# Kernel optimization log

Measured on AMD Instinct MI355X. Metric: run time of the kernel, lower is better.

## Reference

```python
import jax, jax.numpy as jnp
import numpy as np

ROI_SIZE = 7
SPATIAL_SCALE = 1.0 / 16.0
CHUNK = 16  # rois processed per lax.map step to bound the masked-max intermediate


def roi_pool(x, indices_and_rois):
    """Caffe-style RoI max pooling. x: [N,C,H,W]; indices_and_rois: [R,5]=(idx,x1,y1,x2,y2)."""
    N, C, H, W = x.shape
    P = ROI_SIZE
    hi = jnp.arange(H, dtype=x.dtype)
    wi = jnp.arange(W, dtype=x.dtype)
    p = jnp.arange(P, dtype=x.dtype)

    def pool_one(r5):
        idx = r5[0].astype(jnp.int32)
        xmin, ymin, xmax, ymax = r5[1], r5[2], r5[3], r5[4]
        sw = jnp.round(xmin * SPATIAL_SCALE)
        sh = jnp.round(ymin * SPATIAL_SCALE)
        ew = jnp.round(xmax * SPATIAL_SCALE)
        eh = jnp.round(ymax * SPATIAL_SCALE)
        bw = jnp.maximum(ew - sw + 1.0, 1.0) / P  # bin width in feature cells
        bh = jnp.maximum(eh - sh + 1.0, 1.0) / P
        wstart = jnp.clip(jnp.floor(p * bw) + sw, 0.0, float(W))
        wend = jnp.clip(jnp.ceil((p + 1.0) * bw) + sw, 0.0, float(W))
        hstart = jnp.clip(jnp.floor(p * bh) + sh, 0.0, float(H))
        hend = jnp.clip(jnp.ceil((p + 1.0) * bh) + sh, 0.0, float(H))
        colmask = (wi[None, :] >= wstart[:, None]) & (wi[None, :] < wend[:, None])  # [P,W]
        rowmask = (hi[None, :] >= hstart[:, None]) & (hi[None, :] < hend[:, None])  # [P,H]
        img = x[idx]  # [C,H,W] gather of the roi's image
        neg = jnp.asarray(-jnp.inf, x.dtype)
        # max over columns within each column-bin, then over rows within each row-bin
        m1 = jnp.max(jnp.where(colmask[None, None, :, :], img[:, :, None, :], neg), axis=-1)  # [C,H,P]
        m2 = jnp.max(jnp.where(rowmask[None, :, :, None], m1[:, None, :, :], neg), axis=2)  # [C,P,P]
        return jnp.where(jnp.isfinite(m2), m2, jnp.zeros((), x.dtype))  # empty bins -> 0

    R = indices_and_rois.shape[0]
    chunks = indices_and_rois.reshape(R // CHUNK, CHUNK, 5)
    pooled = jax.lax.map(jax.vmap(pool_one), chunks)  # [R//CHUNK, CHUNK, C, P, P]
    return pooled.reshape(R, C, P, P)


def setup_inputs() -> dict:
    key = jax.random.key(0)
    ks = jax.random.split(key, 8)
    N, C, H, W = 4, 512, 50, 50  # 800x800 image, VGG16 stride 16
    R, n_class = 512, 21
    x = jax.random.normal(ks[0], (N, C, H, W), jnp.float32)
    yx1 = jax.random.uniform(ks[1], (R, 2), jnp.float32, 0.0, 700.0)
    wh = jax.random.uniform(ks[2], (R, 2), jnp.float32, 32.0, 128.0)
    rois = jnp.concatenate([yx1, jnp.minimum(yx1 + wh, 799.0)], axis=1)  # (y1,x1,y2,x2)
    roi_indices = jax.random.randint(ks[3], (R,), 0, N)
    din = C * ROI_SIZE * ROI_SIZE
    W1 = jax.random.normal(ks[4], (din, 4096), jnp.float32) * 0.01
    b1 = jnp.zeros((4096,), jnp.float32)
    W2 = jax.random.normal(ks[5], (4096, 4096), jnp.float32) * 0.01
    b2 = jnp.zeros((4096,), jnp.float32)
    Wc = jax.random.normal(ks[6], (4096, n_class * 4), jnp.float32) * 0.001
    bc = jnp.zeros((n_class * 4,), jnp.float32)
    Ws = jax.random.normal(ks[7], (4096, n_class), jnp.float32) * 0.01
    bs = jnp.zeros((n_class,), jnp.float32)
    return {"x": x, "rois": rois, "roi_indices": roi_indices, "W1": W1, "b1": b1,
            "W2": W2, "b2": b2, "Wc": Wc, "bc": bc, "Ws": Ws, "bs": bs}


def reference(x, rois, roi_indices, W1, b1, W2, b2, Wc, bc, Ws, bs):
    # concat index + boxes, then reorder (idx,y1,x1,y2,x2) -> (idx,x1,y1,x2,y2)
    ir = jnp.concatenate([roi_indices[:, None].astype(jnp.float32), rois], axis=1)
    ir = ir[:, jnp.array([0, 2, 1, 4, 3])]
    pool = roi_pool(x, ir)  # [R, C, 7, 7]
    flat = pool.reshape(pool.shape[0], -1)  # [R, 25088]
    fc6 = jax.nn.relu(flat @ W1 + b1)
    fc7 = jax.nn.relu(fc6 @ W2 + b2)
    roi_cls_locs = fc7 @ Wc + bc  # [R, n_class*4]
    roi_scores = fc7 @ Ws + bs  # [R, n_class]
    return (roi_cls_locs, roi_scores)
```

## Files before the change

### kernel.cpp

```cpp
#include <hip/hip_runtime.h>
#include <math.h>

typedef __attribute__((ext_vector_type(8))) short short8;
typedef __attribute__((ext_vector_type(4))) short s16x4;
typedef __attribute__((ext_vector_type(4))) float f32x4;
typedef __attribute__((ext_vector_type(4))) unsigned u32x4;

#define R_ROIS 512
#define CCH 512
#define HH 50
#define WW 50
#define PPOOL 7
#define KDIM (CCH * PPOOL * PPOOL)
#define NH 4096
#define ZSPLIT 8
#define NHEAD 105

#define BARRIER_NO_VMDRAIN()                              \
  do {                                                    \
    asm volatile("s_waitcnt lgkmcnt(0)" ::: "memory");    \
    __builtin_amdgcn_s_barrier();                         \
  } while (0)

__device__ __forceinline__ short f2bf(float f) {
  unsigned u = __builtin_bit_cast(unsigned, f);
  u += 0x7FFFu + ((u >> 16) & 1u);
  return (short)(u >> 16);
}
__device__ __forceinline__ float bf2f(short s) {
  unsigned u = ((unsigned)(unsigned short)s) << 16;
  return __builtin_bit_cast(float, u);
}
__device__ __forceinline__ unsigned cvtpk(float lo, float hi) {
  unsigned r;
  asm("v_cvt_pk_bf16_f32 %0, %1, %2" : "=v"(r) : "v"(lo), "v"(hi));
  return r;
}

__global__ __launch_bounds__(256) void roi_pool_kernel(
    const float* __restrict__ x, const float* __restrict__ rois,
    const int* __restrict__ ridx, short* __restrict__ A) {
  __shared__ int hs[PPOOL], he[PPOOL], wss[PPOOL], wee[PPOOL];
  __shared__ int sidx;
  const int r = blockIdx.x;
  if (threadIdx.x == 0) {
    float ymin = rois[r * 4 + 0], xmin = rois[r * 4 + 1];
    float ymax = rois[r * 4 + 2], xmax = rois[r * 4 + 3];
    float sw = rintf(xmin * 0.0625f);
    float sh = rintf(ymin * 0.0625f);
    float ew = rintf(xmax * 0.0625f);
    float eh = rintf(ymax * 0.0625f);
    float bw = fmaxf(ew - sw + 1.0f, 1.0f) * (1.0f / 7.0f);
    float bh = fmaxf(eh - sh + 1.0f, 1.0f) * (1.0f / 7.0f);
    for (int p = 0; p < PPOOL; ++p) {
      wss[p] = (int)fminf(fmaxf(floorf(p * bw) + sw, 0.0f), 50.0f);
      wee[p] = (int)fminf(fmaxf(ceilf((p + 1) * bw) + sw, 0.0f), 50.0f);
      hs[p]  = (int)fminf(fmaxf(floorf(p * bh) + sh, 0.0f), 50.0f);
      he[p]  = (int)fminf(fmaxf(ceilf((p + 1) * bh) + sh, 0.0f), 50.0f);
    }
    sidx = ridx[r];
  }
  __syncthreads();
  const float* xb = x + (size_t)sidx * CCH * HH * WW;
  const int obeg = blockIdx.y * (KDIM / 8), oend = obeg + KDIM / 8;
  for (int o = obeg + threadIdx.x; o < oend; o += 256) {
    int c = o / 49;
    int pq = o - c * 49;
    int ph = pq / 7, pw = pq - ph * 7;
    const float* xc = xb + (size_t)c * (HH * WW);
    int h0 = hs[ph], h1 = he[ph], w0 = wss[pw], w1 = wee[pw];
    float mv = -INFINITY;
    for (int h = h0; h < h1; ++h) {
      const float* xr = xc + h * WW;
      for (int w = w0; w < w1; ++w) mv = fmaxf(mv, xr[w]);
    }
    A[(size_t)r * KDIM + o] = f2bf((h1 > h0 && w1 > w0) ? mv : 0.0f);
  }
}

__global__ __launch_bounds__(512, 2) void gemm_splitk_kernel(
    const short* __restrict__ A, const float* __restrict__ B,
    float* __restrict__ part, int M, int N, int K, int Ks, int nblk) {
  __shared__ __align__(16) char As[2][256 * 64];
  __shared__ __align__(16) char Bs[2][256 * 64];
  const int bid = blockIdx.x;
  const int vid = (bid & 7) * (nblk >> 3) + (bid >> 3);
  const int mb = vid & 1;
  const int nb = (vid >> 1) & 15;
  const int zb = vid >> 5;
  const int m0 = mb * 256, n0 = nb * 256;
  const int kbeg = zb * Ks;
  const int S = Ks >> 5;
  const int t = threadIdx.x;
  const int lane = t & 63, wid = t >> 6;
  const int wm = wid >> 2, wn = wid & 3;
  const int lr = lane & 15, kc = lane >> 4;
  const int ar = t >> 1, ah = t & 1;
  const int bn = t & 255, bko = t >> 8;

  const short* aptrA = A + (size_t)(m0 + ar) * K + ah * 16;
  const float* bbase = B + n0 + bn;

  const int awz0 = (ar * 64 + ah * 32) ^ ((ar & 7) << 4);
  const int awz1 = awz0 ^ 16;
  const int bwz0 = (bn * 64 + bko * 32) ^ ((bn & 7) << 4);
  const int bwz1 = bwz0 ^ 16;
  const int aoff = (wm * 8192 + lr * 64 + kc * 16) ^ ((lr & 7) << 4);
  const int boff = (wn * 4096 + lr * 64 + kc * 16) ^ ((lr & 7) << 4);

  f32x4 acc[8][4] = {};
  short8 aA0, aA1, aB0, aB1;
  float bA[16], bB[16];

  auto LOADT = [&](int k0, short8& r0, short8& r1, float* br) {
    r0 = *(const short8*)(aptrA + k0);
    r1 = *(const short8*)(aptrA + k0 + 8);
    const float* bp = bbase + (size_t)(k0 + bko * 16) * N;
    #pragma unroll
    for (int j = 0; j < 16; ++j) br[j] = bp[(size_t)j * N];
  };
  auto WRITET = [&](int buf, const short8& r0, const short8& r1, const float* br) {
    *(short8*)(As[buf] + awz0) = r0;
    *(short8*)(As[buf] + awz1) = r1;
    u32x4 w0, w1;
    w0[0] = cvtpk(br[0], br[1]);   w0[1] = cvtpk(br[2], br[3]);
    w0[2] = cvtpk(br[4], br[5]);   w0[3] = cvtpk(br[6], br[7]);
    w1[0] = cvtpk(br[8], br[9]);   w1[1] = cvtpk(br[10], br[11]);
    w1[2] = cvtpk(br[12], br[13]); w1[3] = cvtpk(br[14], br[15]);
    *(u32x4*)(Bs[buf] + bwz0) = w0;
    *(u32x4*)(Bs[buf] + bwz1) = w1;
  };
  auto COMPUTE = [&](int buf) {
    short8 b[4];
    #pragma unroll
    for (int n = 0; n < 4; ++n)
      b[n] = *(const short8*)(Bs[buf] + boff + n * 1024);
    #pragma unroll
    for (int m = 0; m < 8; ++m) {
      short8 a = *(const short8*)(As[buf] + aoff + m * 1024);
      #pragma unroll
      for (int n = 0; n < 4; ++n)
        acc[m][n] = __builtin_amdgcn_mfma_f32_16x16x32_bf16(a, b[n], acc[m][n], 0, 0, 0);
    }
  };

  LOADT(kbeg, aA0, aA1, bA);
  WRITET(0, aA0, aA1, bA);
  LOADT(kbeg + 32, aB0, aB1, bB);
  BARRIER_NO_VMDRAIN();

  int cur = 0;
  for (int i = 0; i < S; i += 2) {
    if (i + 2 < S) LOADT(kbeg + (i + 2) * 32, aA0, aA1, bA);
    COMPUTE(cur);
    WRITET(cur ^ 1, aB0, aB1, bB);
    BARRIER_NO_VMDRAIN();
    cur ^= 1;
    if (i + 3 < S) LOADT(kbeg + (i + 3) * 32, aB0, aB1, bB);
    COMPUTE(cur);
    if (i + 2 < S) {
      WRITET(cur ^ 1, aA0, aA1, bA);
      BARRIER_NO_VMDRAIN();
      cur ^= 1;
    }
  }

  float* pz = part + (size_t)zb * M * N;
  #pragma unroll
  for (int m = 0; m < 8; ++m) {
    #pragma unroll
    for (int n = 0; n < 4; ++n) {
      int col = n0 + wn * 64 + n * 16 + lr;
      #pragma unroll
      for (int j = 0; j < 4; ++j) {
        int row = m0 + wm * 128 + m * 16 + kc * 4 + j;
        pz[(size_t)row * N + col] = acc[m][n][j];
      }
    }
  }
}

__global__ __launch_bounds__(256) void reduce_relu_kernel(
    const float* __restrict__ part, const float* __restrict__ bias,
    short* __restrict__ out, int MN, int N) {
  int i = (blockIdx.x * 256 + threadIdx.x) * 4;
  if (i >= MN) return;
  const float4 b = *(const float4*)(bias + (i & (N - 1)));
  float4 s = *(const float4*)(part + i);
  #pragma unroll
  for (int z = 1; z < ZSPLIT; ++z) {
    float4 p = *(const float4*)(part + (size_t)z * MN + i);
    s.x += p.x; s.y += p.y; s.z += p.z; s.w += p.w;
  }
  s16x4 o;
  o.x = f2bf(fmaxf(s.x + b.x, 0.0f));
  o.y = f2bf(fmaxf(s.y + b.y, 0.0f));
  o.z = f2bf(fmaxf(s.z + b.z, 0.0f));
  o.w = f2bf(fmaxf(s.w + b.w, 0.0f));
  *(s16x4*)(out + i) = o;
}

__global__ __launch_bounds__(256) void pack_head_w_kernel(
    const float* __restrict__ Wc, const float* __restrict__ Wsv,
    short* __restrict__ Wt) {
  const int n = blockIdx.x;
  for (int k = threadIdx.x; k < NH; k += 256) {
    float v = 0.0f;
    if (n < 84) v = Wc[(size_t)k * 84 + n];
    else if (n < NHEAD) v = Wsv[(size_t)k * 21 + (n - 84)];
    Wt[(size_t)n * NH + k] = f2bf(v);
  }
}

__global__ __launch_bounds__(256, 2) void gemm_head_kernel(
    const short* __restrict__ A, const short* __restrict__ Bt,
    float* __restrict__ part2) {
  __shared__ __align__(16) char As[2][128 * 64];
  __shared__ __align__(16) char Bs[2][128 * 64];
  const int m0 = blockIdx.x * 128;
  const int zb = blockIdx.y;
  const int kbeg = zb * (NH / ZSPLIT), kend = kbeg + NH / ZSPLIT;
  const int t = threadIdx.x;
  const int lane = t & 63, wid = t >> 6;
  const int wm = wid >> 1, wn = wid & 1;
  const int lr = lane & 15, kc = lane >> 4;
  const int sr = t >> 2, seg = t & 3;

  const short* aptr0 = A + (size_t)(m0 + sr) * NH + seg * 8;
  const short* aptr1 = aptr0 + (size_t)64 * NH;
  const short* bptr0 = Bt + (size_t)sr * NH + seg * 8;
  const short* bptr1 = bptr0 + (size_t)64 * NH;

  const int wz0 = (sr * 64 + seg * 16) ^ ((sr & 7) << 4);
  const int wz1 = wz0 + 4096;
  const int aoff = (wm * 4096 + lr * 64 + kc * 16) ^ ((lr & 7) << 4);
  const int boff = (wn * 4096 + lr * 64 + kc * 16) ^ ((lr & 7) << 4);

  f32x4 acc[4][4] = {};
  short8 a_r0, a_r1, b_r0, b_r1;

  auto LOADT = [&](int k0) {
    a_r0 = *(const short8*)(aptr0 + k0);
    a_r1 = *(const short8*)(aptr1 + k0);
    b_r0 = *(const short8*)(bptr0 + k0);
    b_r1 = *(const short8*)(bptr1 + k0);
  };
  auto WRITET = [&](int buf) {
    *(short8*)(As[buf] + wz0) = a_r0;
    *(short8*)(As[buf] + wz1) = a_r1;
    *(short8*)(Bs[buf] + wz0) = b_r0;
    *(short8*)(Bs[buf] + wz1) = b_r1;
  };
  auto COMPUTE = [&](int buf) {
    short8 a[4], b[4];
    #pragma unroll
    for (int m = 0; m < 4; ++m)
      a[m] = *(const short8*)(As[buf] + aoff + m * 1024);
    #pragma unroll
    for (int n = 0; n < 4; ++n)
      b[n] = *(const short8*)(Bs[buf] + boff + n * 1024);
    #pragma unroll
    for (int m = 0; m < 4; ++m)
      #pragma unroll
      for (int n = 0; n < 4; ++n)
        acc[m][n] = __builtin_amdgcn_mfma_f32_16x16x32_bf16(a[m], b[n], acc[m][n], 0, 0, 0);
  };

  LOADT(kbeg);
  WRITET(0);
  BARRIER_NO_VMDRAIN();

  int cur = 0;
  for (int k0 = kbeg + 32; k0 <= kend; k0 += 32) {
    bool more = (k0 < kend);
    if (more) LOADT(k0);
    COMPUTE(cur);
    if (more) {
      WRITET(cur ^ 1);
      BARRIER_NO_VMDRAIN();
      cur ^= 1;
    }
  }

  float* pz = part2 + (size_t)zb * R_ROIS * 128;
  #pragma unroll
  for (int m = 0; m < 4; ++m) {
    #pragma unroll
    for (int n = 0; n < 4; ++n) {
      int col = wn * 64 + n * 16 + lr;
      #pragma unroll
      for (int j = 0; j < 4; ++j) {
        int row = m0 + wm * 64 + m * 16 + kc * 4 + j;
        pz[(size_t)row * 128 + col] = acc[m][n][j];
      }
    }
  }
}

__global__ __launch_bounds__(128) void reduce_head_kernel(
    const float* __restrict__ part2, const float* __restrict__ bc,
    const float* __restrict__ bs, float* __restrict__ out) {
  const int r = blockIdx.x, c = threadIdx.x;
  if (c >= NHEAD) return;
  float s = 0.0f;
  #pragma unroll
  for (int z = 0; z < ZSPLIT; ++z)
    s += part2[(size_t)z * R_ROIS * 128 + (size_t)r * 128 + c];
  if (c < 84)
    out[(size_t)r * 84 + c] = s + bc[c];
  else
    out[(size_t)R_ROIS * 84 + (size_t)r * 21 + (c - 84)] = s + bs[c - 84];
}

extern "C" void kernel_launch(void* const* d_in, const int* in_sizes, int n_in,
                              void* d_out, int out_size, void* d_ws, size_t ws_size,
                              hipStream_t stream) {
  const float* x    = (const float*)d_in[0];
  const float* rois = (const float*)d_in[1];
  const int*   ridx = (const int*)d_in[2];
  const float* W1   = (const float*)d_in[3];
  const float* b1   = (const float*)d_in[4];
  const float* W2   = (const float*)d_in[5];
  const float* b2   = (const float*)d_in[6];
  const float* Wc   = (const float*)d_in[7];
  const float* bc   = (const float*)d_in[8];
  const float* Wsv  = (const float*)d_in[9];
  const float* bs   = (const float*)d_in[10];

  const int MN = R_ROIS * NH;
  short* A     = (short*)d_ws;
  short* fc6   = A + (size_t)R_ROIS * KDIM;
  short* fc7   = fc6 + (size_t)MN;
  float* part  = (float*)(fc7 + (size_t)MN);
  float* part2 = part + (size_t)ZSPLIT * MN;
  short* Wt    = (short*)(part2 + (size_t)ZSPLIT * R_ROIS * 128);

  roi_pool_kernel<<<dim3(R_ROIS, 8), 256, 0, stream>>>(x, rois, ridx, A);
  pack_head_w_kernel<<<128, 256, 0, stream>>>(Wc, Wsv, Wt);

  gemm_splitk_kernel<<<256, 512, 0, stream>>>(A, W1, part, R_ROIS, NH, KDIM,
                                              KDIM / ZSPLIT, 256);
  reduce_relu_kernel<<<MN / 4 / 256, 256, 0, stream>>>(part, b1, fc6, MN, NH);

  gemm_splitk_kernel<<<256, 512, 0, stream>>>(fc6, W2, part, R_ROIS, NH, NH,
                                              NH / ZSPLIT, 256);
  reduce_relu_kernel<<<MN / 4 / 256, 256, 0, stream>>>(part, b2, fc7, MN, NH);

  gemm_head_kernel<<<dim3(4, ZSPLIT), 256, 0, stream>>>(fc7, Wt, part2);
  reduce_head_kernel<<<R_ROIS, 128, 0, stream>>>(part2, bc, bs, (float*)d_out);
}
```

Measured before the change: 294.1 us.

## Use 128x128-tile split-K=2 GEMM for fc7 layer

Adds a new GEMM kernel with 128x128 tiles, 256 threads and double-buffered LDS, and uses it for the fc7 matmul with split-K reduced from 8 to 2. The fc7 layer gets 256 blocks of smaller tiles with longer K loops in place of many deep splits. This cuts the partial-sum traffic written and then reduced, since the reduce kernel now sums only 2 partials. In exchange each block runs a longer serial K loop, and the smaller tiles reuse operands less.

```diff
diff --git a/kernel.cpp b/kernel.cpp
--- a/kernel.cpp
+++ b/kernel.cpp
@@ -14,6 +14,7 @@
 #define KDIM (CCH * PPOOL * PPOOL)
 #define NH 4096
 #define ZSPLIT 8
+#define ZF7 2
 #define NHEAD 105
 
 #define BARRIER_NO_VMDRAIN()                              \
@@ -180,15 +181,117 @@
   }
 }
 
+__global__ __launch_bounds__(256, 2) void gemm128_splitk_kernel(
+    const short* __restrict__ A, const float* __restrict__ B,
+    float* __restrict__ part, int M, int N, int K, int Ks, int nblk) {
+  __shared__ __align__(16) char As[2][128 * 64];
+  __shared__ __align__(16) char Bs[2][128 * 64];
+  const int bid = blockIdx.x;
+  const int vid = (bid & 7) * (nblk >> 3) + (bid >> 3);
+  const int mb = vid & 3;
+  const int nb = (vid >> 2) & 31;
+  const int zb = vid >> 7;
+  const int m0 = mb * 128, n0 = nb * 128;
+  const int kbeg = zb * Ks;
+  const int S = Ks >> 5;
+  const int t = threadIdx.x;
+  const int lane = t & 63, wid = t >> 6;
+  const int wm = wid >> 1, wn = wid & 1;
+  const int lr = lane & 15, kc = lane >> 4;
+  const int ar = t >> 1, ah = t & 1;
+  const int bn = t & 127, bkh = t >> 7;
+
+  const short* aptrA = A + (size_t)(m0 + ar) * K + ah * 16;
+  const float* bbase = B + n0 + bn;
+
+  const int awz0 = (ar * 64 + ah * 32) ^ ((ar & 7) << 4);
+  const int awz1 = awz0 ^ 16;
+  const int bwz0 = (bn * 64 + bkh * 32) ^ ((bn & 7) << 4);
+  const int bwz1 = bwz0 ^ 16;
+  const int aoff = (wm * 4096 + lr * 64 + kc * 16) ^ ((lr & 7) << 4);
+  const int boff = (wn * 4096 + lr * 64 + kc * 16) ^ ((lr & 7) << 4);
+
+  f32x4 acc[4][4] = {};
+  short8 aA0, aA1, aB0, aB1;
+  float bA[16], bB[16];
+
+  auto LOADT = [&](int k0, short8& r0, short8& r1, float* br) {
+    r0 = *(const short8*)(aptrA + k0);
+    r1 = *(const short8*)(aptrA + k0 + 8);
+    const float* bp = bbase + (size_t)(k0 + bkh * 16) * N;
+    #pragma unroll
+    for (int j = 0; j < 16; ++j) br[j] = bp[(size_t)j * N];
+  };
+  auto WRITET = [&](int buf, const short8& r0, const short8& r1, const float* br) {
+    *(short8*)(As[buf] + awz0) = r0;
+    *(short8*)(As[buf] + awz1) = r1;
+    u32x4 w0, w1;
+    w0[0] = cvtpk(br[0], br[1]);   w0[1] = cvtpk(br[2], br[3]);
+    w0[2] = cvtpk(br[4], br[5]);   w0[3] = cvtpk(br[6], br[7]);
+    w1[0] = cvtpk(br[8], br[9]);   w1[1] = cvtpk(br[10], br[11]);
+    w1[2] = cvtpk(br[12], br[13]); w1[3] = cvtpk(br[14], br[15]);
+    *(u32x4*)(Bs[buf] + bwz0) = w0;
+    *(u32x4*)(Bs[buf] + bwz1) = w1;
+  };
+  auto COMPUTE = [&](int buf) {
+    short8 a[4], b[4];
+    #pragma unroll
+    for (int m = 0; m < 4; ++m)
+      a[m] = *(const short8*)(As[buf] + aoff + m * 1024);
+    #pragma unroll
+    for (int n = 0; n < 4; ++n)
+      b[n] = *(const short8*)(Bs[buf] + boff + n * 1024);
+    #pragma unroll
+    for (int m = 0; m < 4; ++m)
+      #pragma unroll
+      for (int n = 0; n < 4; ++n)
+        acc[m][n] = __builtin_amdgcn_mfma_f32_16x16x32_bf16(a[m], b[n], acc[m][n], 0, 0, 0);
+  };
+
+  LOADT(kbeg, aA0, aA1, bA);
+  WRITET(0, aA0, aA1, bA);
+  LOADT(kbeg + 32, aB0, aB1, bB);
+  BARRIER_NO_VMDRAIN();
+
+  int cur = 0;
+  for (int i = 0; i < S; i += 2) {
+    if (i + 2 < S) LOADT(kbeg + (i + 2) * 32, aA0, aA1, bA);
+    COMPUTE(cur);
+    WRITET(cur ^ 1, aB0, aB1, bB);
+    BARRIER_NO_VMDRAIN();
+    cur ^= 1;
+    if (i + 3 < S) LOADT(kbeg + (i + 3) * 32, aB0, aB1, bB);
+    COMPUTE(cur);
+    if (i + 2 < S) {
+      WRITET(cur ^ 1, aA0, aA1, bA);
+      BARRIER_NO_VMDRAIN();
+      cur ^= 1;
+    }
+  }
+
+  float* pz = part + (size_t)zb * M * N;
+  #pragma unroll
+  for (int m = 0; m < 4; ++m) {
+    #pragma unroll
+    for (int n = 0; n < 4; ++n) {
+      int col = n0 + wn * 64 + n * 16 + lr;
+      #pragma unroll
+      for (int j = 0; j < 4; ++j) {
+        int row = m0 + wm * 64 + m * 16 + kc * 4 + j;
+        pz[(size_t)row * N + col] = acc[m][n][j];
+      }
+    }
+  }
+}
+
 __global__ __launch_bounds__(256) void reduce_relu_kernel(
     const float* __restrict__ part, const float* __restrict__ bias,
-    short* __restrict__ out, int MN, int N) {
+    short* __restrict__ out, int MN, int N, int Z) {
   int i = (blockIdx.x * 256 + threadIdx.x) * 4;
   if (i >= MN) return;
   const float4 b = *(const float4*)(bias + (i & (N - 1)));
   float4 s = *(const float4*)(part + i);
-  #pragma unroll
-  for (int z = 1; z < ZSPLIT; ++z) {
+  for (int z = 1; z < Z; ++z) {
     float4 p = *(const float4*)(part + (size_t)z * MN + i);
     s.x += p.x; s.y += p.y; s.z += p.z; s.w += p.w;
   }
@@ -340,11 +443,11 @@
 
   gemm_splitk_kernel<<<256, 512, 0, stream>>>(A, W1, part, R_ROIS, NH, KDIM,
                                               KDIM / ZSPLIT, 256);
-  reduce_relu_kernel<<<MN / 4 / 256, 256, 0, stream>>>(part, b1, fc6, MN, NH);
-
-  gemm_splitk_kernel<<<256, 512, 0, stream>>>(fc6, W2, part, R_ROIS, NH, NH,
-                                              NH / ZSPLIT, 256);
-  reduce_relu_kernel<<<MN / 4 / 256, 256, 0, stream>>>(part, b2, fc7, MN, NH);
+  reduce_relu_kernel<<<MN / 4 / 256, 256, 0, stream>>>(part, b1, fc6, MN, NH, ZSPLIT);
+
+  gemm128_splitk_kernel<<<256, 256, 0, stream>>>(fc6, W2, part, R_ROIS, NH, NH,
+                                                 NH / ZF7, 256);
+  reduce_relu_kernel<<<MN / 4 / 256, 256, 0, stream>>>(part, b2, fc7, MN, NH, ZF7);
 
   gemm_head_kernel<<<dim3(4, ZSPLIT), 256, 0, stream>>>(fc7, Wt, part2);
   reduce_head_kernel<<<R_ROIS, 128, 0, stream>>>(part2, bc, bs, (float*)d_out);
```

Result: no change. 299.9 us (+2.0%).
